# Performance work log

Hardware: AMD Instinct MI355X
Metric: run time of the kernel (lower is better)

Reference implementation:

```python
import jax, jax.numpy as jnp
import numpy as np

D_MODEL = 1024
N_HEADS = 16
D_HEAD = D_MODEL // N_HEADS
D_FF = 4096
EPS = 1e-6  # flax LayerNorm default


def setup_inputs() -> dict:
    key = jax.random.key(0)
    ks = jax.random.split(key, 16)
    s = 1.0 / np.sqrt(D_MODEL)
    inp = {
        'x':  jax.random.normal(ks[0], (4, 2048, D_MODEL), jnp.float32),
        'Wq': jax.random.normal(ks[1], (D_MODEL, D_MODEL), jnp.float32) * s,
        'bq': jnp.zeros((D_MODEL,), jnp.float32),
        'Wk': jax.random.normal(ks[2], (D_MODEL, D_MODEL), jnp.float32) * s,
        'bk': jnp.zeros((D_MODEL,), jnp.float32),
        'Wv': jax.random.normal(ks[3], (D_MODEL, D_MODEL), jnp.float32) * s,
        'bv': jnp.zeros((D_MODEL,), jnp.float32),
        'Wo': jax.random.normal(ks[4], (D_MODEL, D_MODEL), jnp.float32) * s,
        'W1': jax.random.normal(ks[5], (D_MODEL, D_FF), jnp.float32) * s,
        'b1': jnp.zeros((D_FF,), jnp.float32),
        'W2': jax.random.normal(ks[6], (D_FF, D_MODEL), jnp.float32) * (1.0 / np.sqrt(D_FF)),
        'b2': jnp.zeros((D_MODEL,), jnp.float32),
        'g1': jnp.ones((D_MODEL,), jnp.float32),
        'beta1': jnp.zeros((D_MODEL,), jnp.float32),
        'g2': jnp.ones((D_MODEL,), jnp.float32),
        'beta2': jnp.zeros((D_MODEL,), jnp.float32),
    }
    return inp


def _layernorm(x, g, b):
    mu = jnp.mean(x, axis=-1, keepdims=True)
    var = jnp.mean(jnp.square(x - mu), axis=-1, keepdims=True)
    return (x - mu) * jax.lax.rsqrt(var + EPS) * g + b


def _attention(x, Wq, bq, Wk, bk, Wv, bv, Wo):
    B, S, D = x.shape
    def split_heads(t):
        return t.reshape(B, S, N_HEADS, D_HEAD).transpose(0, 2, 1, 3)  # bhsd
    q = split_heads(x @ Wq + bq)
    k = split_heads(x @ Wk + bk)
    v = split_heads(x @ Wv + bv)
    scale = jnp.sqrt(jnp.float32(D_HEAD))
    scores = jnp.einsum('bhsd,bhtd->bhst', q, k) / scale
    causal = jnp.tril(jnp.ones((S, S), dtype=jnp.bool_))
    scores = jnp.where(causal, scores, jnp.finfo(scores.dtype).min)
    w = jax.nn.softmax(scores, axis=-1)
    out = jnp.einsum('bhst,bhtd->bhsd', w, v)
    out = out.transpose(0, 2, 1, 3).reshape(B, S, D)
    return out @ Wo  # o_proj has no bias


def reference(x, Wq, bq, Wk, bk, Wv, bv, Wo, W1, b1, W2, b2, g1, beta1, g2, beta2):
    normed = _layernorm(x, g1, beta1)
    x = x + _attention(normed, Wq, bq, Wk, bk, Wv, bv, Wo)
    normed = _layernorm(x, g2, beta2)
    h = jax.nn.gelu(normed @ W1 + b1)  # approximate tanh gelu, matching flax nn.gelu
    x = x + (h @ W2 + b2)
    return x
```

## Files before the change

### kernel.cpp

```cpp
#include <hip/hip_runtime.h>

#define SEQ 2048
#define NROWS 8192
#define NH 16
#define DHEAD 64
#define QLD 3072

typedef float f32x4 __attribute__((ext_vector_type(4)));
typedef __bf16 bf16x8 __attribute__((ext_vector_type(8)));

__device__ __forceinline__ unsigned short f2bf(float f) {
  union { float f; unsigned u; } v; v.f = f;
  unsigned r = v.u + 0x7fffu + ((v.u >> 16) & 1u);
  return (unsigned short)(r >> 16);
}

__device__ __forceinline__ void gl16(const void* g, void* l) {
  __builtin_amdgcn_global_load_lds((const __attribute__((address_space(1))) void*)g,
                                   (__attribute__((address_space(3))) void*)l, 16, 0, 0);
}

__device__ __forceinline__ float gelu_f(float x) {
  float t = 0.7978845608028654f * (x + 0.044715f * x * x * x);
  float e = __expf(2.0f * t);
  float th = 1.0f - 2.0f / (e + 1.0f);
  return 0.5f * x * (1.0f + th);
}

#define CVTPK(dst, lo, hi) asm("v_cvt_pk_bf16_f32 %0, %1, %2" : "=v"(dst) : "v"(lo), "v"(hi))

#if __has_builtin(__builtin_amdgcn_permlane32_swap)
#define P32SWAP(a, b, x, y) { auto _t = __builtin_amdgcn_permlane32_swap((a), (b), false, false); (x) = _t[0]; (y) = _t[1]; }
#else
#define P32SWAP(a, b, x, y) { unsigned _as = (unsigned)__shfl_xor((int)(a), 32, 64); \
  unsigned _bs = (unsigned)__shfl_xor((int)(b), 32, 64); \
  (x) = (l < 32) ? (a) : _bs; (y) = (l < 32) ? _as : (b); }
#endif
#if __has_builtin(__builtin_amdgcn_permlane16_swap)
#define P16SWAP(a, b, x, y) { auto _t = __builtin_amdgcn_permlane16_swap((a), (b), false, false); (x) = _t[0]; (y) = _t[1]; }
#else
#define P16SWAP(a, b, x, y) { unsigned _as = (unsigned)__shfl_xor((int)(a), 16, 64); \
  unsigned _bs = (unsigned)__shfl_xor((int)(b), 16, 64); \
  (x) = (l & 16) ? _bs : (a); (y) = (l & 16) ? (b) : _as; }
#endif

#define MEMFENCE asm volatile("" ::: "memory")
#define BAR() do { MEMFENCE; __builtin_amdgcn_s_barrier(); MEMFENCE; } while (0)
#define WAIT_LGKM0 asm volatile("s_waitcnt lgkmcnt(0)" ::: "memory")
#define WAIT_VM0 asm volatile("s_waitcnt vmcnt(0)" ::: "memory")

__global__ __launch_bounds__(256) void transpose_cvt(const float* __restrict__ W,
                                                     unsigned short* __restrict__ Wt,
                                                     int K, int N) {
  __shared__ float tile[32][33];
  const int tx = threadIdx.x, ty = threadIdx.y;
  const int n0 = blockIdx.x * 32, k0 = blockIdx.y * 32;
#pragma unroll
  for (int i = ty; i < 32; i += 8)
    tile[i][tx] = W[(size_t)(k0 + i) * N + n0 + tx];
  __syncthreads();
#pragma unroll
  for (int i = ty; i < 32; i += 8)
    Wt[(size_t)(n0 + i) * K + k0 + tx] = f2bf(tile[tx][i]);
}

__global__ __launch_bounds__(256) void concat_bias(const float* __restrict__ bq,
                                                   const float* __restrict__ bk,
                                                   const float* __restrict__ bv,
                                                   float* __restrict__ dst) {
  int i = blockIdx.x * 256 + threadIdx.x;
  if (i < 1024) dst[i] = bq[i];
  else if (i < 2048) dst[i] = bk[i - 1024];
  else if (i < 3072) dst[i] = bv[i - 2048];
}

__global__ __launch_bounds__(256) void layernorm_k(const float* __restrict__ x,
                                                   const float* __restrict__ g,
                                                   const float* __restrict__ b,
                                                   unsigned short* __restrict__ out) {
  const int row = blockIdx.x, tid = threadIdx.x;
  const float4 v = reinterpret_cast<const float4*>(x + (size_t)row * 1024)[tid];
  float s = v.x + v.y + v.z + v.w;
  float s2 = v.x * v.x + v.y * v.y + v.z * v.z + v.w * v.w;
#pragma unroll
  for (int d = 1; d < 64; d <<= 1) { s += __shfl_xor(s, d, 64); s2 += __shfl_xor(s2, d, 64); }
  __shared__ float ls[4], ls2[4];
  const int w = tid >> 6;
  if ((tid & 63) == 0) { ls[w] = s; ls2[w] = s2; }
  __syncthreads();
  s = ls[0] + ls[1] + ls[2] + ls[3];
  s2 = ls2[0] + ls2[1] + ls2[2] + ls2[3];
  const float mu = s * (1.0f / 1024.0f);
  const float var = s2 * (1.0f / 1024.0f) - mu * mu;
  const float rstd = rsqrtf(var + 1e-6f);
  const float4 gv = reinterpret_cast<const float4*>(g)[tid];
  const float4 bv = reinterpret_cast<const float4*>(b)[tid];
  ushort4 o;
  o.x = f2bf((v.x - mu) * rstd * gv.x + bv.x);
  o.y = f2bf((v.y - mu) * rstd * gv.y + bv.y);
  o.z = f2bf((v.z - mu) * rstd * gv.z + bv.z);
  o.w = f2bf((v.w - mu) * rstd * gv.w + bv.w);
  reinterpret_cast<ushort4*>(out + (size_t)row * 1024)[tid] = o;
}

enum { EP_BIAS = 1, EP_RES = 2, EP_GELU = 4, EP_BF16 = 8, EP_QSCALE = 16 };

template <int BM, int E>
__global__ __launch_bounds__(512, 2) void gemm8_k(const unsigned short* __restrict__ A,
                                                  const unsigned short* __restrict__ Bt,
                                                  const float* __restrict__ bias,
                                                  const float* __restrict__ resid,
                                                  void* __restrict__ out,
                                                  int M, int N, int K) {
  constexpr int BN = 256;
  constexpr int WM = BM / 2;
  constexpr int MI = WM / 16;
  constexpr int MQ = MI / 2;
  __shared__ __align__(16) unsigned short As[2][BM * 64];
  __shared__ __align__(16) unsigned short Bs[2][BN * 64];

  const int tid = threadIdx.x;
  const int l = tid & 63, w = tid >> 6;
  const int lr = l & 15, lg = l >> 4;
  const int wr = w >> 2, wc = w & 3;

  const int gx = gridDim.x;
  const int nwg = gx * gridDim.y;
  int lin = blockIdx.y * gx + blockIdx.x;
  lin = (lin & 7) * (nwg >> 3) + (lin >> 3);
  const int bn = lin % gx, bm = lin / gx;

  const unsigned short* Ab = A + (size_t)(bm * BM) * K;
  const unsigned short* Bb = Bt + (size_t)(bn * BN) * K;

  const int srow8 = l >> 3;
  const int slot = (l & 7) ^ (srow8 & 7);
  auto stA = [&](int buf, int t, int s) {
    gl16((const char*)(Ab + (size_t)(s * 8 + srow8) * K + t * 64) + slot * 16,
         (char*)(&As[buf][0]) + s * 1024 + l * 16);
  };
  auto stB = [&](int buf, int t, int s) {
    gl16((const char*)(Bb + (size_t)(s * 8 + srow8) * K + t * 64) + slot * 16,
         (char*)(&Bs[buf][0]) + s * 1024 + l * 16);
  };
  auto stageAll = [&](int buf, int t) {
    stA(buf, t, w); stA(buf, t, 8 + w);
    if (BM == 256) { stA(buf, t, 16 + w); stA(buf, t, 24 + w); }
    stB(buf, t, w); stB(buf, t, 8 + w); stB(buf, t, 16 + w); stB(buf, t, 24 + w);
  };
  auto rdA = [&](int buf, int r, int ks) {
    return *reinterpret_cast<const bf16x8*>(
        (const char*)(&As[buf][0]) + r * 128 + (((ks << 2) + lg) ^ (r & 7)) * 16);
  };
  auto rdB = [&](int buf, int r, int ks) {
    return *reinterpret_cast<const bf16x8*>(
        (const char*)(&Bs[buf][0]) + r * 128 + (((ks << 2) + lg) ^ (r & 7)) * 16);
  };

  f32x4 acc[MI][4];
#pragma unroll
  for (int m = 0; m < MI; ++m)
#pragma unroll
    for (int n = 0; n < 4; ++n) acc[m][n] = 0.0f;

  const int NK = K >> 6;
  stageAll(0, 0);
  WAIT_VM0;
  BAR();

#pragma unroll 2
  for (int kt = 0; kt < NK; ++kt) {
    const int c = kt & 1, nb = c ^ 1;
    const bool more = kt + 1 < NK;
    bf16x8 a0[MQ][2], a1[MQ][2], b0[2][2], b1[2][2];

    if (more) stageAll(nb, kt + 1);
#pragma unroll
    for (int mi = 0; mi < MQ; ++mi)
#pragma unroll
      for (int ks = 0; ks < 2; ++ks) a0[mi][ks] = rdA(c, wr * WM + mi * 16 + lr, ks);
#pragma unroll
    for (int ni = 0; ni < 2; ++ni)
#pragma unroll
      for (int ks = 0; ks < 2; ++ks) b0[ni][ks] = rdB(c, wc * 64 + ni * 16 + lr, ks);
    BAR();
    WAIT_LGKM0;
    __builtin_amdgcn_s_setprio(1);
#pragma unroll
    for (int mi = 0; mi < MQ; ++mi)
#pragma unroll
      for (int ni = 0; ni < 2; ++ni)
#pragma unroll
        for (int ks = 0; ks < 2; ++ks)
          acc[mi][ni] = __builtin_amdgcn_mfma_f32_16x16x32_bf16(a0[mi][ks], b0[ni][ks], acc[mi][ni], 0, 0, 0);
    __builtin_amdgcn_s_setprio(0);
    BAR();

#pragma unroll
    for (int ni = 0; ni < 2; ++ni)
#pragma unroll
      for (int ks = 0; ks < 2; ++ks) b1[ni][ks] = rdB(c, wc * 64 + (2 + ni) * 16 + lr, ks);
    BAR();
    WAIT_LGKM0;
    __builtin_amdgcn_s_setprio(1);
#pragma unroll
    for (int mi = 0; mi < MQ; ++mi)
#pragma unroll
      for (int ni = 0; ni < 2; ++ni)
#pragma unroll
        for (int ks = 0; ks < 2; ++ks)
          acc[mi][2 + ni] = __builtin_amdgcn_mfma_f32_16x16x32_bf16(a0[mi][ks], b1[ni][ks], acc[mi][2 + ni], 0, 0, 0);
    __builtin_amdgcn_s_setprio(0);
    BAR();

#pragma unroll
    for (int mi = 0; mi < MQ; ++mi)
#pragma unroll
      for (int ks = 0; ks < 2; ++ks) a1[mi][ks] = rdA(c, wr * WM + (MQ + mi) * 16 + lr, ks);
    BAR();
    WAIT_LGKM0;
    __builtin_amdgcn_s_setprio(1);
#pragma unroll
    for (int mi = 0; mi < MQ; ++mi)
#pragma unroll
      for (int ni = 0; ni < 2; ++ni)
#pragma unroll
        for (int ks = 0; ks < 2; ++ks)
          acc[MQ + mi][ni] = __builtin_amdgcn_mfma_f32_16x16x32_bf16(a1[mi][ks], b0[ni][ks], acc[MQ + mi][ni], 0, 0, 0);
    __builtin_amdgcn_s_setprio(0);
    BAR();

    __builtin_amdgcn_s_setprio(1);
#pragma unroll
    for (int mi = 0; mi < MQ; ++mi)
#pragma unroll
      for (int ni = 0; ni < 2; ++ni)
#pragma unroll
        for (int ks = 0; ks < 2; ++ks)
          acc[MQ + mi][2 + ni] = __builtin_amdgcn_mfma_f32_16x16x32_bf16(a1[mi][ks], b1[ni][ks], acc[MQ + mi][2 + ni], 0, 0, 0);
    __builtin_amdgcn_s_setprio(0);
    WAIT_VM0;
    BAR();
  }

  const int row0 = bm * BM + wr * WM;
  const int col0 = bn * BN + wc * 64;
#pragma unroll
  for (int m = 0; m < MI; ++m) {
#pragma unroll
    for (int n = 0; n < 4; ++n) {
      const int col = col0 + n * 16 + lr;
      float bc = 0.0f;
      if (E & EP_BIAS) bc = bias[col];
#pragma unroll
      for (int j = 0; j < 4; ++j) {
        const int row = row0 + m * 16 + lg * 4 + j;
        float v = acc[m][n][j] + bc;
        if (E & EP_RES) v += resid[(size_t)row * N + col];
        if (E & EP_GELU) v = gelu_f(v);
        if (E & EP_QSCALE) { if (col < 1024) v *= 0.18033688011112042f; }
        if (E & EP_BF16) ((unsigned short*)out)[(size_t)row * N + col] = f2bf(v);
        else ((float*)out)[(size_t)row * N + col] = v;
      }
    }
  }
}

__global__ __launch_bounds__(512, 4) void attn_k(const unsigned short* __restrict__ qkv,
                                                 unsigned short* __restrict__ out) {
  __shared__ __align__(16) unsigned short Kl[2][128 * 64];
  __shared__ __align__(16) unsigned short Vt[2][64 * 128];
  const int tid = threadIdx.x;
  const int l = tid & 63, w = tid >> 6;
  const int lr = l & 15, lg = l >> 4;
  const int bh = blockIdx.y;
  const int b = bh >> 4, h = bh & 15;
  const size_t rowbase = (size_t)b * SEQ;
  char* klb = (char*)Kl;
  char* vtb = (char*)Vt;

  const int srow8 = l >> 3;
  const int kslot = (l & 7) ^ (srow8 & 7);
  auto stageK = [&](int buf, int kb2) {
#pragma unroll
    for (int s = w; s < 16; s += 8) {
      const char* src = (const char*)(qkv + (rowbase + kb2 + s * 8 + srow8) * QLD + 1024 + h * 64)
                        + kslot * 16;
      gl16(src, klb + buf * 16384 + s * 1024 + l * 16);
    }
  };
  const int sg = tid & 31, dhg = tid >> 5;
  auto loadV = [&](int kb2, uint2* vr) {
#pragma unroll
    for (int i = 0; i < 4; ++i)
      vr[i] = *reinterpret_cast<const uint2*>(
          qkv + (rowbase + kb2 + sg * 4 + i) * QLD + 2048 + h * 64 + dhg * 4);
  };
  auto writeV = [&](int buf, const uint2* vr) {
    char* vb = vtb + buf * 16384;
#pragma unroll
    for (int jj = 0; jj < 4; ++jj) {
      const int dh = dhg * 4 + jj;
      unsigned a0 = (jj < 2) ? vr[0].x : vr[0].y;
      unsigned a1 = (jj < 2) ? vr[1].x : vr[1].y;
      unsigned a2 = (jj < 2) ? vr[2].x : vr[2].y;
      unsigned a3 = (jj < 2) ? vr[3].x : vr[3].y;
      unsigned s01, s23;
      if (jj & 1) {
        s01 = (a0 >> 16) | (a1 & 0xffff0000u);
        s23 = (a2 >> 16) | (a3 & 0xffff0000u);
      } else {
        s01 = (a0 & 0xffffu) | (a1 << 16);
        s23 = (a2 & 0xffffu) | (a3 << 16);
      }
      const int bo = dh * 256 + (((sg >> 1) ^ (dh & 15)) << 4) + ((sg & 1) << 3);
      uint2 p; p.x = s01; p.y = s23;
      *reinterpret_cast<uint2*>(vb + bo) = p;
    }
  };

#pragma unroll 1
  for (int seg = 0; seg < 2; ++seg) {
    const int qt = seg ? (15 - blockIdx.x) : blockIdx.x;
    const int q0 = qt << 7;
    const int qwmin = q0 + w * 16;
    const int qrow = qwmin + lr;

    bf16x8 qf[2];
#pragma unroll
    for (int ks = 0; ks < 2; ++ks)
      qf[ks] = *reinterpret_cast<const bf16x8*>(
          qkv + (rowbase + qrow) * QLD + h * 64 + ks * 32 + lg * 8);

    f32x4 oacc[4];
#pragma unroll
    for (int n = 0; n < 4; ++n) oacc[n] = 0.0f;
    float mrun = -1e30f, lrun = 0.0f;

    {
      stageK(0, 0);
      uint2 vr0[4];
      loadV(0, vr0);
      writeV(0, vr0);
    }
    __syncthreads();

#pragma unroll 1
    for (int kt = 0; kt <= qt; ++kt) {
      const int cur = kt & 1, nb = cur ^ 1;
      const int kb = kt << 7;
      const bool more = kt < qt;
      uint2 vr[4];
      if (more) { stageK(nb, kb + 128); loadV(kb + 128, vr); }

      f32x4 sacc[8];
#pragma unroll
      for (int ni = 0; ni < 8; ++ni) sacc[ni] = 0.0f;
      const char* kc = klb + cur * 16384;
      __builtin_amdgcn_s_setprio(1);
#pragma unroll
      for (int ks = 0; ks < 2; ++ks) {
#pragma unroll
        for (int ni = 0; ni < 8; ++ni) {
          const int r = ni * 16 + lr;
          const int bo = r * 128 + ((((ks << 2) + lg) ^ (r & 7)) << 4);
          bf16x8 kf = *reinterpret_cast<const bf16x8*>(kc + bo);
          sacc[ni] = __builtin_amdgcn_mfma_f32_16x16x32_bf16(kf, qf[ks], sacc[ni], 0, 0, 0);
        }
      }
      __builtin_amdgcn_s_setprio(0);

      if (kt == qt) {
#pragma unroll
        for (int ni = 0; ni < 8; ++ni)
#pragma unroll
          for (int j = 0; j < 4; ++j)
            if (kb + ni * 16 + lg * 4 + j > qrow) sacc[ni][j] = -1e30f;
      }

      float pm = sacc[0][0];
#pragma unroll
      for (int ni = 0; ni < 8; ++ni)
#pragma unroll
        for (int j = 0; j < 4; ++j) pm = fmaxf(pm, sacc[ni][j]);
      pm = fmaxf(pm, __shfl_xor(pm, 16, 64));
      pm = fmaxf(pm, __shfl_xor(pm, 32, 64));
      if (!__all(pm <= mrun + 8.0f)) {
        const float mnew = fmaxf(mrun, pm);
        const float alpha = exp2f(mrun - mnew);
        mrun = mnew;
        lrun *= alpha;
#pragma unroll
        for (int n = 0; n < 4; ++n) oacc[n] *= alpha;
      }
      float rs = 0.0f;
#pragma unroll
      for (int ni = 0; ni < 8; ++ni)
#pragma unroll
        for (int j = 0; j < 4; ++j) {
          const float p = exp2f(sacc[ni][j] - mrun);
          sacc[ni][j] = p;
          rs += p;
        }
      rs += __shfl_xor(rs, 16, 64);
      rs += __shfl_xor(rs, 32, 64);
      lrun += rs;

      if (more) writeV(nb, vr);

      const char* vc = vtb + cur * 16384;
#pragma unroll
      for (int g = 0; g < 4; ++g) {
        unsigned U0, U1, U2, U3, C0, C1, W0, W1, W2, W3;
        CVTPK(U0, sacc[2 * g][0], sacc[2 * g][1]);
        CVTPK(U1, sacc[2 * g][2], sacc[2 * g][3]);
        CVTPK(U2, sacc[2 * g + 1][0], sacc[2 * g + 1][1]);
        CVTPK(U3, sacc[2 * g + 1][2], sacc[2 * g + 1][3]);
        P32SWAP(U0, U2, C0, C1);
        P16SWAP(C0, C1, W0, W2);
        P32SWAP(U1, U3, C0, C1);
        P16SWAP(C0, C1, W1, W3);
        union { uint4 u; bf16x8 v; } pu;
        pu.u = make_uint4(W0, W1, W2, W3);
        __builtin_amdgcn_s_setprio(1);
#pragma unroll
        for (int n = 0; n < 4; ++n) {
          const int r = n * 16 + lr;
          const int bo = r * 256 + ((((g << 2) + lg) ^ (r & 15)) << 4);
          bf16x8 vf = *reinterpret_cast<const bf16x8*>(vc + bo);
          oacc[n] = __builtin_amdgcn_mfma_f32_16x16x32_bf16(vf, pu.v, oacc[n], 0, 0, 0);
        }
        __builtin_amdgcn_s_setprio(0);
      }
      __syncthreads();
    }

    const float inv = 1.0f / lrun;
#pragma unroll
    for (int n = 0; n < 4; ++n) {
      ushort4 o;
      o.x = f2bf(oacc[n][0] * inv);
      o.y = f2bf(oacc[n][1] * inv);
      o.z = f2bf(oacc[n][2] * inv);
      o.w = f2bf(oacc[n][3] * inv);
      *reinterpret_cast<ushort4*>(out + (rowbase + qrow) * 1024 + h * 64 + n * 16 + lg * 4) = o;
    }
  }
}

extern "C" void kernel_launch(void* const* d_in, const int* in_sizes, int n_in,
                              void* d_out, int out_size, void* d_ws, size_t ws_size,
                              hipStream_t stream) {
  const float* x   = (const float*)d_in[0];
  const float* Wq  = (const float*)d_in[1];
  const float* bq  = (const float*)d_in[2];
  const float* Wk  = (const float*)d_in[3];
  const float* bk  = (const float*)d_in[4];
  const float* Wv  = (const float*)d_in[5];
  const float* bv  = (const float*)d_in[6];
  const float* Wo  = (const float*)d_in[7];
  const float* W1  = (const float*)d_in[8];
  const float* b1  = (const float*)d_in[9];
  const float* W2  = (const float*)d_in[10];
  const float* b2  = (const float*)d_in[11];
  const float* g1  = (const float*)d_in[12];
  const float* be1 = (const float*)d_in[13];
  const float* g2  = (const float*)d_in[14];
  const float* be2 = (const float*)d_in[15];

  char* ws = (char*)d_ws;
  size_t off = 0;
  auto alloc = [&](size_t bytes) { char* p = ws + off; off += (bytes + 255) & ~(size_t)255; return p; };
  unsigned short* WqkvT = (unsigned short*)alloc((size_t)3072 * 1024 * 2);
  unsigned short* WoT   = (unsigned short*)alloc((size_t)1024 * 1024 * 2);
  unsigned short* W1T   = (unsigned short*)alloc((size_t)4096 * 1024 * 2);
  unsigned short* W2T   = (unsigned short*)alloc((size_t)1024 * 4096 * 2);
  float*          bqkv  = (float*)alloc((size_t)3072 * 4);
  unsigned short* normed = (unsigned short*)alloc((size_t)NROWS * 1024 * 2);
  unsigned short* qkvbuf = (unsigned short*)alloc((size_t)NROWS * 4096 * 2);
  unsigned short* attnb  = (unsigned short*)alloc((size_t)NROWS * 1024 * 2);
  float*          x1     = (float*)alloc((size_t)NROWS * 1024 * 4);

  const dim3 tb(32, 8);
  transpose_cvt<<<dim3(32, 32), tb, 0, stream>>>(Wq, WqkvT, 1024, 1024);
  transpose_cvt<<<dim3(32, 32), tb, 0, stream>>>(Wk, WqkvT + 1024 * 1024, 1024, 1024);
  transpose_cvt<<<dim3(32, 32), tb, 0, stream>>>(Wv, WqkvT + 2 * 1024 * 1024, 1024, 1024);
  transpose_cvt<<<dim3(32, 32), tb, 0, stream>>>(Wo, WoT, 1024, 1024);
  transpose_cvt<<<dim3(128, 32), tb, 0, stream>>>(W1, W1T, 1024, 4096);
  transpose_cvt<<<dim3(32, 128), tb, 0, stream>>>(W2, W2T, 4096, 1024);
  concat_bias<<<12, 256, 0, stream>>>(bq, bk, bv, bqkv);

  layernorm_k<<<NROWS, 256, 0, stream>>>(x, g1, be1, normed);
  gemm8_k<256, (EP_BIAS | EP_BF16 | EP_QSCALE)><<<dim3(12, 32), 512, 0, stream>>>(normed, WqkvT, bqkv, nullptr, qkvbuf, NROWS, 3072, 1024);
  attn_k<<<dim3(8, 64), 512, 0, stream>>>(qkvbuf, attnb);
  gemm8_k<128, EP_RES><<<dim3(4, 64), 512, 0, stream>>>(attnb, WoT, nullptr, x, x1, NROWS, 1024, 1024);
  layernorm_k<<<NROWS, 256, 0, stream>>>(x1, g2, be2, normed);
  gemm8_k<256, (EP_BIAS | EP_GELU | EP_BF16)><<<dim3(16, 32), 512, 0, stream>>>(normed, W1T, b1, nullptr, qkvbuf, NROWS, 4096, 1024);
  gemm8_k<128, (EP_BIAS | EP_RES)><<<dim3(4, 64), 512, 0, stream>>>(qkvbuf, W2T, b2, x1, d_out, NROWS, 1024, 4096);
}
```

Before: 596.0 us.

## Replace GEMM with triple-buffered 256x128 tile kernel using partial vmcnt waits

Replaces the double-buffered gemm8 kernel (BM up to 256, BN=256, several barriers per k-step) with gemm3_k. The new kernel uses a 256x128 tile, 4x2 warps each owning a 64x64 subtile, and a three-slot LDS ring. Loads are issued two k-steps ahead and waited on with vmcnt(6), leaving one barrier per iteration. This aims to hide global-load latency and cut barrier overhead, at the cost of 144KB LDS per block and smaller N tiles, which means more re-reads of A. The attention kernel's launch-bounds occupancy hint also drops from 4 to 2.

```diff
diff --git a/kernel.cpp b/kernel.cpp
--- a/kernel.cpp
+++ b/kernel.cpp
@@ -47,6 +47,7 @@
 #define MEMFENCE asm volatile("" ::: "memory")
 #define BAR() do { MEMFENCE; __builtin_amdgcn_s_barrier(); MEMFENCE; } while (0)
 #define WAIT_LGKM0 asm volatile("s_waitcnt lgkmcnt(0)" ::: "memory")
+#define WAIT_VM6 asm volatile("s_waitcnt vmcnt(6)" ::: "memory")
 #define WAIT_VM0 asm volatile("s_waitcnt vmcnt(0)" ::: "memory")
 
 __global__ __launch_bounds__(256) void transpose_cvt(const float* __restrict__ W,
@@ -105,24 +106,18 @@
 
 enum { EP_BIAS = 1, EP_RES = 2, EP_GELU = 4, EP_BF16 = 8, EP_QSCALE = 16 };
 
-template <int BM, int E>
-__global__ __launch_bounds__(512, 2) void gemm8_k(const unsigned short* __restrict__ A,
-                                                  const unsigned short* __restrict__ Bt,
-                                                  const float* __restrict__ bias,
-                                                  const float* __restrict__ resid,
-                                                  void* __restrict__ out,
-                                                  int M, int N, int K) {
-  constexpr int BN = 256;
-  constexpr int WM = BM / 2;
-  constexpr int MI = WM / 16;
-  constexpr int MQ = MI / 2;
-  __shared__ __align__(16) unsigned short As[2][BM * 64];
-  __shared__ __align__(16) unsigned short Bs[2][BN * 64];
-
+template <int E>
+__global__ __launch_bounds__(512) void gemm3_k(const unsigned short* __restrict__ A,
+                                               const unsigned short* __restrict__ Bt,
+                                               const float* __restrict__ bias,
+                                               const float* __restrict__ resid,
+                                               void* __restrict__ out,
+                                               int M, int N, int K) {
+  __shared__ __align__(16) unsigned short Ls[3][24576];
   const int tid = threadIdx.x;
   const int l = tid & 63, w = tid >> 6;
   const int lr = l & 15, lg = l >> 4;
-  const int wr = w >> 2, wc = w & 3;
+  const int wr = w >> 1, wc = w & 1;
 
   const int gx = gridDim.x;
   const int nwg = gx * gridDim.y;
@@ -130,123 +125,76 @@
   lin = (lin & 7) * (nwg >> 3) + (lin >> 3);
   const int bn = lin % gx, bm = lin / gx;
 
-  const unsigned short* Ab = A + (size_t)(bm * BM) * K;
-  const unsigned short* Bb = Bt + (size_t)(bn * BN) * K;
+  const unsigned short* Ab = A + (size_t)(bm * 256) * K;
+  const unsigned short* Bb = Bt + (size_t)(bn * 128) * K;
+  const int NK = K >> 6;
 
   const int srow8 = l >> 3;
-  const int slot = (l & 7) ^ (srow8 & 7);
-  auto stA = [&](int buf, int t, int s) {
-    gl16((const char*)(Ab + (size_t)(s * 8 + srow8) * K + t * 64) + slot * 16,
-         (char*)(&As[buf][0]) + s * 1024 + l * 16);
+  const int sslot = (l & 7) ^ srow8;
+  const size_t rs8 = (size_t)8 * K * 2;
+
+  auto stage = [&](int slot, int t) {
+    if (t >= NK) return;
+    char* base = (char*)(&Ls[slot][0]);
+    const char* a0 = (const char*)(Ab + (size_t)srow8 * K + t * 64) + sslot * 16;
+    const char* b0 = (const char*)(Bb + (size_t)srow8 * K + t * 64) + sslot * 16;
+    gl16(a0 + (size_t)w * rs8,        base + w * 1024 + l * 16);
+    gl16(a0 + (size_t)(8 + w) * rs8,  base + (8 + w) * 1024 + l * 16);
+    gl16(a0 + (size_t)(16 + w) * rs8, base + (16 + w) * 1024 + l * 16);
+    gl16(a0 + (size_t)(24 + w) * rs8, base + (24 + w) * 1024 + l * 16);
+    gl16(b0 + (size_t)w * rs8,        base + 32768 + w * 1024 + l * 16);
+    gl16(b0 + (size_t)(8 + w) * rs8,  base + 32768 + (8 + w) * 1024 + l * 16);
   };
-  auto stB = [&](int buf, int t, int s) {
-    gl16((const char*)(Bb + (size_t)(s * 8 + srow8) * K + t * 64) + slot * 16,
-         (char*)(&Bs[buf][0]) + s * 1024 + l * 16);
+  auto rd = [&](const char* base, int r, int ks) {
+    return *reinterpret_cast<const bf16x8*>(base + r * 128 + (((ks << 2) + lg) ^ (r & 7)) * 16);
   };
-  auto stageAll = [&](int buf, int t) {
-    stA(buf, t, w); stA(buf, t, 8 + w);
-    if (BM == 256) { stA(buf, t, 16 + w); stA(buf, t, 24 + w); }
-    stB(buf, t, w); stB(buf, t, 8 + w); stB(buf, t, 16 + w); stB(buf, t, 24 + w);
-  };
-  auto rdA = [&](int buf, int r, int ks) {
-    return *reinterpret_cast<const bf16x8*>(
-        (const char*)(&As[buf][0]) + r * 128 + (((ks << 2) + lg) ^ (r & 7)) * 16);
-  };
-  auto rdB = [&](int buf, int r, int ks) {
-    return *reinterpret_cast<const bf16x8*>(
-        (const char*)(&Bs[buf][0]) + r * 128 + (((ks << 2) + lg) ^ (r & 7)) * 16);
-  };
-
-  f32x4 acc[MI][4];
-#pragma unroll
-  for (int m = 0; m < MI; ++m)
+
+  f32x4 acc[4][4];
+#pragma unroll
+  for (int m = 0; m < 4; ++m)
 #pragma unroll
     for (int n = 0; n < 4; ++n) acc[m][n] = 0.0f;
 
-  const int NK = K >> 6;
-  stageAll(0, 0);
-  WAIT_VM0;
-  BAR();
-
-#pragma unroll 2
-  for (int kt = 0; kt < NK; ++kt) {
-    const int c = kt & 1, nb = c ^ 1;
-    const bool more = kt + 1 < NK;
-    bf16x8 a0[MQ][2], a1[MQ][2], b0[2][2], b1[2][2];
-
-    if (more) stageAll(nb, kt + 1);
-#pragma unroll
-    for (int mi = 0; mi < MQ; ++mi)
-#pragma unroll
-      for (int ks = 0; ks < 2; ++ks) a0[mi][ks] = rdA(c, wr * WM + mi * 16 + lr, ks);
-#pragma unroll
-    for (int ni = 0; ni < 2; ++ni)
-#pragma unroll
-      for (int ks = 0; ks < 2; ++ks) b0[ni][ks] = rdB(c, wc * 64 + ni * 16 + lr, ks);
+  stage(0, 0);
+  stage(1, 1);
+  int cs = 0, ss = 2;
+
+  for (int t = 0; t < NK; ++t) {
+    if (t + 1 < NK) { WAIT_VM6; } else { WAIT_VM0; }
     BAR();
+    stage(ss, t + 2);
+
+    const char* Ac = (const char*)(&Ls[cs][0]);
+    const char* Bc = Ac + 32768;
+    bf16x8 af[4][2], bf[4][2];
+#pragma unroll
+    for (int mi = 0; mi < 4; ++mi)
+#pragma unroll
+      for (int ks = 0; ks < 2; ++ks) af[mi][ks] = rd(Ac, wr * 64 + mi * 16 + lr, ks);
+#pragma unroll
+    for (int ni = 0; ni < 4; ++ni)
+#pragma unroll
+      for (int ks = 0; ks < 2; ++ks) bf[ni][ks] = rd(Bc, wc * 64 + ni * 16 + lr, ks);
+
+    __builtin_amdgcn_s_setprio(1);
+#pragma unroll
+    for (int mi = 0; mi < 4; ++mi)
+#pragma unroll
+      for (int ni = 0; ni < 4; ++ni)
+#pragma unroll
+        for (int ks = 0; ks < 2; ++ks)
+          acc[mi][ni] = __builtin_amdgcn_mfma_f32_16x16x32_bf16(af[mi][ks], bf[ni][ks], acc[mi][ni], 0, 0, 0);
+    __builtin_amdgcn_s_setprio(0);
     WAIT_LGKM0;
-    __builtin_amdgcn_s_setprio(1);
-#pragma unroll
-    for (int mi = 0; mi < MQ; ++mi)
-#pragma unroll
-      for (int ni = 0; ni < 2; ++ni)
-#pragma unroll
-        for (int ks = 0; ks < 2; ++ks)
-          acc[mi][ni] = __builtin_amdgcn_mfma_f32_16x16x32_bf16(a0[mi][ks], b0[ni][ks], acc[mi][ni], 0, 0, 0);
-    __builtin_amdgcn_s_setprio(0);
-    BAR();
-
-#pragma unroll
-    for (int ni = 0; ni < 2; ++ni)
-#pragma unroll
-      for (int ks = 0; ks < 2; ++ks) b1[ni][ks] = rdB(c, wc * 64 + (2 + ni) * 16 + lr, ks);
-    BAR();
-    WAIT_LGKM0;
-    __builtin_amdgcn_s_setprio(1);
-#pragma unroll
-    for (int mi = 0; mi < MQ; ++mi)
-#pragma unroll
-      for (int ni = 0; ni < 2; ++ni)
-#pragma unroll
-        for (int ks = 0; ks < 2; ++ks)
-          acc[mi][2 + ni] = __builtin_amdgcn_mfma_f32_16x16x32_bf16(a0[mi][ks], b1[ni][ks], acc[mi][2 + ni], 0, 0, 0);
-    __builtin_amdgcn_s_setprio(0);
-    BAR();
-
-#pragma unroll
-    for (int mi = 0; mi < MQ; ++mi)
-#pragma unroll
-      for (int ks = 0; ks < 2; ++ks) a1[mi][ks] = rdA(c, wr * WM + (MQ + mi) * 16 + lr, ks);
-    BAR();
-    WAIT_LGKM0;
-    __builtin_amdgcn_s_setprio(1);
-#pragma unroll
-    for (int mi = 0; mi < MQ; ++mi)
-#pragma unroll
-      for (int ni = 0; ni < 2; ++ni)
-#pragma unroll
-        for (int ks = 0; ks < 2; ++ks)
-          acc[MQ + mi][ni] = __builtin_amdgcn_mfma_f32_16x16x32_bf16(a1[mi][ks], b0[ni][ks], acc[MQ + mi][ni], 0, 0, 0);
-    __builtin_amdgcn_s_setprio(0);
-    BAR();
-
-    __builtin_amdgcn_s_setprio(1);
-#pragma unroll
-    for (int mi = 0; mi < MQ; ++mi)
-#pragma unroll
-      for (int ni = 0; ni < 2; ++ni)
-#pragma unroll
-        for (int ks = 0; ks < 2; ++ks)
-          acc[MQ + mi][2 + ni] = __builtin_amdgcn_mfma_f32_16x16x32_bf16(a1[mi][ks], b1[ni][ks], acc[MQ + mi][2 + ni], 0, 0, 0);
-    __builtin_amdgcn_s_setprio(0);
-    WAIT_VM0;
-    BAR();
+
+    cs = (cs == 2) ? 0 : cs + 1;
+    ss = (ss == 2) ? 0 : ss + 1;
   }
 
-  const int row0 = bm * BM + wr * WM;
-  const int col0 = bn * BN + wc * 64;
-#pragma unroll
-  for (int m = 0; m < MI; ++m) {
+  const int row0 = bm * 256 + wr * 64;
+  const int col0 = bn * 128 + wc * 64;
+#pragma unroll
+  for (int m = 0; m < 4; ++m) {
 #pragma unroll
     for (int n = 0; n < 4; ++n) {
       const int col = col0 + n * 16 + lr;
@@ -266,7 +214,7 @@
   }
 }
 
-__global__ __launch_bounds__(512, 4) void attn_k(const unsigned short* __restrict__ qkv,
+__global__ __launch_bounds__(512, 2) void attn_k(const unsigned short* __restrict__ qkv,
                                                  unsigned short* __restrict__ out) {
   __shared__ __align__(16) unsigned short Kl[2][128 * 64];
   __shared__ __align__(16) unsigned short Vt[2][64 * 128];
@@ -491,10 +439,10 @@
   concat_bias<<<12, 256, 0, stream>>>(bq, bk, bv, bqkv);
 
   layernorm_k<<<NROWS, 256, 0, stream>>>(x, g1, be1, normed);
-  gemm8_k<256, (EP_BIAS | EP_BF16 | EP_QSCALE)><<<dim3(12, 32), 512, 0, stream>>>(normed, WqkvT, bqkv, nullptr, qkvbuf, NROWS, 3072, 1024);
+  gemm3_k<(EP_BIAS | EP_BF16 | EP_QSCALE)><<<dim3(24, 32), 512, 0, stream>>>(normed, WqkvT, bqkv, nullptr, qkvbuf, NROWS, 3072, 1024);
   attn_k<<<dim3(8, 64), 512, 0, stream>>>(qkvbuf, attnb);
-  gemm8_k<128, EP_RES><<<dim3(4, 64), 512, 0, stream>>>(attnb, WoT, nullptr, x, x1, NROWS, 1024, 1024);
+  gemm3_k<EP_RES><<<dim3(8, 32), 512, 0, stream>>>(attnb, WoT, nullptr, x, x1, NROWS, 1024, 1024);
   layernorm_k<<<NROWS, 256, 0, stream>>>(x1, g2, be2, normed);
-  gemm8_k<256, (EP_BIAS | EP_GELU | EP_BF16)><<<dim3(16, 32), 512, 0, stream>>>(normed, W1T, b1, nullptr, qkvbuf, NROWS, 4096, 1024);
-  gemm8_k<128, (EP_BIAS | EP_RES)><<<dim3(4, 64), 512, 0, stream>>>(qkvbuf, W2T, b2, x1, d_out, NROWS, 1024, 4096);
-}
+  gemm3_k<(EP_BIAS | EP_GELU | EP_BF16)><<<dim3(32, 32), 512, 0, stream>>>(normed, W1T, b1, nullptr, qkvbuf, NROWS, 4096, 1024);
+  gemm3_k<(EP_BIAS | EP_RES)><<<dim3(8, 32), 512, 0, stream>>>(qkvbuf, W2T, b2, x1, d_out, NROWS, 1024, 4096);
+}
```

New measurement: 542.2 us. -9.0%, faster.
